# Performance work log

Measured on AMD Instinct MI355X. Metric: run time of the kernel, lower is better.

Reference implementation:

```python
import jax, jax.numpy as jnp
import numpy as np
import math

CLASSES = 1024
IN_F = 32
OUT_F = 32
N = 262144


def setup_inputs() -> dict:
    key = jax.random.key(0)
    k1, k2, k3, k4 = jax.random.split(key, 4)
    k = math.sqrt(1.0 / float(IN_F))
    inp = jax.random.normal(k1, (N, IN_F), dtype=jnp.float32)
    inds = jax.random.randint(k2, (N,), 0, CLASSES, dtype=jnp.int32)
    w = jax.random.uniform(k3, (CLASSES, IN_F, OUT_F), dtype=jnp.float32, minval=-k, maxval=k)
    b = jax.random.uniform(k4, (CLASSES, 1, OUT_F), dtype=jnp.float32, minval=-k, maxval=k)
    return {"input": inp, "inds": inds, "w": w, "b": b}


def reference(input, inds, w, b):
    # per-row expert matmul: out[n] = input[n] @ w[inds[n]] + b[inds[n]]
    w_g = w[inds]            # [n, in, out] gathered expert weights
    b_g = b[inds, 0]         # [n, out]
    return jnp.einsum('ni,nio->no', input, w_g) + b_g
```

## Files before the change

### kernel.cpp

```cpp
#include <hip/hip_runtime.h>


#define N_ROWS      262144
#define N_CLASSES   1024
#define IN_F        32
#define OUT_F       32
#define HB          64
#define ROWS_PER_HB (N_ROWS / HB)

__global__ __launch_bounds__(256) void k_hist(const int* __restrict__ inds,
                                              int* __restrict__ bcT) {
    __shared__ int h[N_CLASSES];
    const int tid = threadIdx.x;
    for (int c = tid; c < N_CLASSES; c += 256) h[c] = 0;
    __syncthreads();
    const int base = blockIdx.x * ROWS_PER_HB;
    for (int k = 0; k < ROWS_PER_HB; k += 256)
        atomicAdd(&h[inds[base + k + tid]], 1);
    __syncthreads();
    for (int c = tid; c < N_CLASSES; c += 256)
        bcT[c * HB + blockIdx.x] = h[c];
}

__global__ __launch_bounds__(1024) void k_scan(const int* __restrict__ bcT,
                                               int* __restrict__ cls_off) {
    __shared__ int s[N_CLASSES];
    const int c = threadIdx.x;
    const int4* p = (const int4*)(bcT + c * HB);
    int total = 0;
#pragma unroll
    for (int j = 0; j < HB / 4; ++j) {
        const int4 t = p[j];
        total += t.x + t.y + t.z + t.w;
    }
    s[c] = total;
    __syncthreads();
    for (int off = 1; off < N_CLASSES; off <<= 1) {
        int v = (c >= off) ? s[c - off] : 0;
        __syncthreads();
        s[c] += v;
        __syncthreads();
    }
    cls_off[c] = s[c] - total;
    if (c == N_CLASSES - 1) cls_off[N_CLASSES] = s[c];
}

__global__ __launch_bounds__(256) void k_offsets(int* __restrict__ bcT,
                                                 const int* __restrict__ cls_off) {
    const int c = blockIdx.x * 256 + threadIdx.x;
    int run = cls_off[c];
    int4* p = (int4*)(bcT + c * HB);
#pragma unroll
    for (int j = 0; j < HB / 4; ++j) {
        const int4 t = p[j];
        int4 o;
        o.x = run; run += t.x;
        o.y = run; run += t.y;
        o.z = run; run += t.z;
        o.w = run; run += t.w;
        p[j] = o;
    }
}

__global__ __launch_bounds__(256) void k_scatter(const int* __restrict__ inds,
                                                 const int* __restrict__ bcT,
                                                 int* __restrict__ rowids) {
    __shared__ int cur[N_CLASSES];
    const int tid = threadIdx.x;
    for (int c = tid; c < N_CLASSES; c += 256)
        cur[c] = bcT[c * HB + blockIdx.x];
    __syncthreads();
    const int base = blockIdx.x * ROWS_PER_HB;
    for (int k = 0; k < ROWS_PER_HB; k += 256) {
        const int row = base + k + tid;
        const int c = inds[row];
        const int pos = atomicAdd(&cur[c], 1);
        rowids[pos] = row;
    }
}

__global__ __launch_bounds__(256) void k_condmul(const float* __restrict__ input,
                                                 const float* __restrict__ w,
                                                 const float* __restrict__ bias,
                                                 const int* __restrict__ rowids,
                                                 const int* __restrict__ cls_off,
                                                 float* __restrict__ out) {
    __shared__ float wlds[IN_F * OUT_F];
    const int cls = blockIdx.x;
    const int tid = threadIdx.x;

    ((float4*)wlds)[tid] = ((const float4*)(w + (size_t)cls * IN_F * OUT_F))[tid];

    const int oq = tid & 7;
    const int rg = tid >> 3;
    const float4 bv = ((const float4*)(bias + (size_t)cls * OUT_F))[oq];
    const int start = cls_off[cls];
    const int count = cls_off[cls + 1] - start;
    __syncthreads();

    const float4* wl4 = (const float4*)wlds;
    const int iters = (count + 31) >> 5;
    for (int it = 0; it < iters; ++it) {
        const int ri = it * 32 + rg;
        const bool valid = ri < count;
        const int idx = valid ? ri : (count - 1);
        const int row = rowids[start + idx];

        const float4* xin = (const float4*)(input + (size_t)row * IN_F);
        float4 x[8];
#pragma unroll
        for (int j = 0; j < 8; ++j) x[j] = xin[j];

        float4 acc = bv;
#pragma unroll
        for (int j = 0; j < 8; ++j) {
            const float a0 = x[j].x, a1 = x[j].y, a2 = x[j].z, a3 = x[j].w;
            const float4 w0 = wl4[(j * 4 + 0) * (OUT_F / 4) + oq];
            const float4 w1 = wl4[(j * 4 + 1) * (OUT_F / 4) + oq];
            const float4 w2 = wl4[(j * 4 + 2) * (OUT_F / 4) + oq];
            const float4 w3 = wl4[(j * 4 + 3) * (OUT_F / 4) + oq];
            acc.x += a0 * w0.x; acc.y += a0 * w0.y; acc.z += a0 * w0.z; acc.w += a0 * w0.w;
            acc.x += a1 * w1.x; acc.y += a1 * w1.y; acc.z += a1 * w1.z; acc.w += a1 * w1.w;
            acc.x += a2 * w2.x; acc.y += a2 * w2.y; acc.z += a2 * w2.z; acc.w += a2 * w2.w;
            acc.x += a3 * w3.x; acc.y += a3 * w3.y; acc.z += a3 * w3.z; acc.w += a3 * w3.w;
        }
        if (valid)
            ((float4*)(out + (size_t)row * OUT_F))[oq] = acc;
    }
}

__global__ __launch_bounds__(256) void k_naive(const float* __restrict__ input,
                                               const int* __restrict__ inds,
                                               const float* __restrict__ w,
                                               const float* __restrict__ bias,
                                               float* __restrict__ out) {
    const int tid = threadIdx.x;
    const int oq = tid & 7;
    const int rg = tid >> 3;
    const int row = blockIdx.x * 32 + rg;
    if (row >= N_ROWS) return;
    const int c = inds[row];
    const float4* xin = (const float4*)(input + (size_t)row * IN_F);
    const float4* wr = (const float4*)(w + (size_t)c * IN_F * OUT_F);
    float4 acc = ((const float4*)(bias + (size_t)c * OUT_F))[oq];
#pragma unroll
    for (int j = 0; j < 8; ++j) {
        const float4 xv = xin[j];
        const float a0 = xv.x, a1 = xv.y, a2 = xv.z, a3 = xv.w;
        const float4 w0 = wr[(j * 4 + 0) * (OUT_F / 4) + oq];
        const float4 w1 = wr[(j * 4 + 1) * (OUT_F / 4) + oq];
        const float4 w2 = wr[(j * 4 + 2) * (OUT_F / 4) + oq];
        const float4 w3 = wr[(j * 4 + 3) * (OUT_F / 4) + oq];
        acc.x += a0 * w0.x; acc.y += a0 * w0.y; acc.z += a0 * w0.z; acc.w += a0 * w0.w;
        acc.x += a1 * w1.x; acc.y += a1 * w1.y; acc.z += a1 * w1.z; acc.w += a1 * w1.w;
        acc.x += a2 * w2.x; acc.y += a2 * w2.y; acc.z += a2 * w2.z; acc.w += a2 * w2.w;
        acc.x += a3 * w3.x; acc.y += a3 * w3.y; acc.z += a3 * w3.z; acc.w += a3 * w3.w;
    }
    ((float4*)(out + (size_t)row * OUT_F))[oq] = acc;
}

extern "C" void kernel_launch(void* const* d_in, const int* in_sizes, int n_in,
                              void* d_out, int out_size, void* d_ws, size_t ws_size,
                              hipStream_t stream) {
    const float* input = (const float*)d_in[0];
    const int*   inds  = (const int*)d_in[1];
    const float* w     = (const float*)d_in[2];
    const float* bias  = (const float*)d_in[3];
    float* out = (float*)d_out;

    int* ws = (int*)d_ws;
    int* bcT     = ws;
    int* cls_off = ws + N_CLASSES * HB;
    int* rowids  = cls_off + N_CLASSES + 1 + 3;
    const size_t need = (size_t)(N_CLASSES * HB + N_CLASSES + 4 + N_ROWS) * sizeof(int);

    if (ws_size >= need) {
        k_hist<<<HB, 256, 0, stream>>>(inds, bcT);
        k_scan<<<1, 1024, 0, stream>>>(bcT, cls_off);
        k_offsets<<<N_CLASSES / 256, 256, 0, stream>>>(bcT, cls_off);
        k_scatter<<<HB, 256, 0, stream>>>(inds, bcT, rowids);
        k_condmul<<<N_CLASSES, 256, 0, stream>>>(input, w, bias, rowids, cls_off, out);
    } else {
        k_naive<<<N_ROWS / 32, 256, 0, stream>>>(input, inds, w, bias, out);
    }
}
```

Measured before the change: 125.2 us.

## Hold expert weights in registers and split the K dimension across thread pairs

The per-class matmul kernel now keeps each thread's slice of the expert weights (16 float4) in registers instead of staging the whole matrix in LDS. The input dimension is split into two halves across thread pairs, with the partial sums combined by a cross-lane shuffle, and the block size doubles to 512 with an occupancy hint. This removes the LDS weight reads and the block barrier from the inner loop. In exchange it raises register pressure, makes redundant global weight loads per thread, and each shuffle adds a cross-lane exchange per row.

```diff
diff --git a/kernel.cpp b/kernel.cpp
--- a/kernel.cpp
+++ b/kernel.cpp
@@ -79,26 +79,29 @@
     }
 }
 
-__global__ __launch_bounds__(256) void k_condmul(const float* __restrict__ input,
-                                                 const float* __restrict__ w,
-                                                 const float* __restrict__ bias,
-                                                 const int* __restrict__ rowids,
-                                                 const int* __restrict__ cls_off,
-                                                 float* __restrict__ out) {
-    __shared__ float wlds[IN_F * OUT_F];
+__global__ __launch_bounds__(512, 4) void k_condmul(const float* __restrict__ input,
+                                                    const float* __restrict__ w,
+                                                    const float* __restrict__ bias,
+                                                    const int* __restrict__ rowids,
+                                                    const int* __restrict__ cls_off,
+                                                    float* __restrict__ out) {
     const int cls = blockIdx.x;
     const int tid = threadIdx.x;
-
-    ((float4*)wlds)[tid] = ((const float4*)(w + (size_t)cls * IN_F * OUT_F))[tid];
-
     const int oq = tid & 7;
-    const int rg = tid >> 3;
-    const float4 bv = ((const float4*)(bias + (size_t)cls * OUT_F))[oq];
+    const int kh = (tid >> 3) & 1;
+    const int rg = tid >> 4;
+
     const int start = cls_off[cls];
     const int count = cls_off[cls + 1] - start;
-    __syncthreads();
-
-    const float4* wl4 = (const float4*)wlds;
+    if (count <= 0) return;
+
+    const float4* w4 = (const float4*)(w + (size_t)cls * (IN_F * OUT_F)) + (size_t)kh * 16 * (OUT_F / 4) + oq;
+    float4 wk[16];
+#pragma unroll
+    for (int j = 0; j < 16; ++j) wk[j] = w4[(size_t)j * (OUT_F / 4)];
+
+    const float4 bv = ((const float4*)(bias + (size_t)cls * OUT_F))[oq];
+
     const int iters = (count + 31) >> 5;
     for (int it = 0; it < iters; ++it) {
         const int ri = it * 32 + rg;
@@ -106,26 +109,37 @@
         const int idx = valid ? ri : (count - 1);
         const int row = rowids[start + idx];
 
-        const float4* xin = (const float4*)(input + (size_t)row * IN_F);
-        float4 x[8];
-#pragma unroll
-        for (int j = 0; j < 8; ++j) x[j] = xin[j];
-
-        float4 acc = bv;
-#pragma unroll
-        for (int j = 0; j < 8; ++j) {
+        const float4* xin = (const float4*)(input + (size_t)row * IN_F + kh * 16);
+        float4 x[4];
+#pragma unroll
+        for (int j = 0; j < 4; ++j) x[j] = xin[j];
+
+        float4 acc = {0.f, 0.f, 0.f, 0.f};
+#pragma unroll
+        for (int j = 0; j < 4; ++j) {
             const float a0 = x[j].x, a1 = x[j].y, a2 = x[j].z, a3 = x[j].w;
-            const float4 w0 = wl4[(j * 4 + 0) * (OUT_F / 4) + oq];
-            const float4 w1 = wl4[(j * 4 + 1) * (OUT_F / 4) + oq];
-            const float4 w2 = wl4[(j * 4 + 2) * (OUT_F / 4) + oq];
-            const float4 w3 = wl4[(j * 4 + 3) * (OUT_F / 4) + oq];
+            const float4 w0 = wk[4 * j + 0];
+            const float4 w1 = wk[4 * j + 1];
+            const float4 w2 = wk[4 * j + 2];
+            const float4 w3 = wk[4 * j + 3];
             acc.x += a0 * w0.x; acc.y += a0 * w0.y; acc.z += a0 * w0.z; acc.w += a0 * w0.w;
             acc.x += a1 * w1.x; acc.y += a1 * w1.y; acc.z += a1 * w1.z; acc.w += a1 * w1.w;
             acc.x += a2 * w2.x; acc.y += a2 * w2.y; acc.z += a2 * w2.z; acc.w += a2 * w2.w;
             acc.x += a3 * w3.x; acc.y += a3 * w3.y; acc.z += a3 * w3.z; acc.w += a3 * w3.w;
         }
-        if (valid)
-            ((float4*)(out + (size_t)row * OUT_F))[oq] = acc;
+        acc.x += __shfl_xor(acc.x, 8);
+        acc.y += __shfl_xor(acc.y, 8);
+        acc.z += __shfl_xor(acc.z, 8);
+        acc.w += __shfl_xor(acc.w, 8);
+
+        if (valid && kh == 0) {
+            float4 o;
+            o.x = acc.x + bv.x;
+            o.y = acc.y + bv.y;
+            o.z = acc.z + bv.z;
+            o.w = acc.w + bv.w;
+            ((float4*)(out + (size_t)row * OUT_F))[oq] = o;
+        }
     }
 }
 
@@ -179,7 +193,7 @@
         k_scan<<<1, 1024, 0, stream>>>(bcT, cls_off);
         k_offsets<<<N_CLASSES / 256, 256, 0, stream>>>(bcT, cls_off);
         k_scatter<<<HB, 256, 0, stream>>>(inds, bcT, rowids);
-        k_condmul<<<N_CLASSES, 256, 0, stream>>>(input, w, bias, rowids, cls_off, out);
+        k_condmul<<<N_CLASSES, 512, 0, stream>>>(input, w, bias, rowids, cls_off, out);
     } else {
         k_naive<<<N_ROWS / 32, 256, 0, stream>>>(input, inds, w, bias, out);
     }
```

Measured after the change: 138.6 us. +10.7%, slower.

## Fuse offsets pass into scan kernel and process two rows per thread

Applied to the files above, without the earlier changes.

Folds the per-block offset computation into the single-block scan kernel, which removes one kernel launch. The condmul kernel now handles two rows per thread per iteration so loads and FMAs from independent rows can overlap, reusing each LDS weight read twice. It also adds an early exit for empty classes. In exchange the fused offset pass runs on one block of 1024 threads instead of four blocks, and register pressure goes up.

```diff
diff --git a/kernel.cpp b/kernel.cpp
--- a/kernel.cpp
+++ b/kernel.cpp
@@ -22,11 +22,11 @@
         bcT[c * HB + blockIdx.x] = h[c];
 }
 
-__global__ __launch_bounds__(1024) void k_scan(const int* __restrict__ bcT,
+__global__ __launch_bounds__(1024) void k_scan(int* __restrict__ bcT,
                                                int* __restrict__ cls_off) {
     __shared__ int s[N_CLASSES];
     const int c = threadIdx.x;
-    const int4* p = (const int4*)(bcT + c * HB);
+    int4* p = (int4*)(bcT + c * HB);
     int total = 0;
 #pragma unroll
     for (int j = 0; j < HB / 4; ++j) {
@@ -41,15 +41,9 @@
         s[c] += v;
         __syncthreads();
     }
-    cls_off[c] = s[c] - total;
+    int run = s[c] - total;
+    cls_off[c] = run;
     if (c == N_CLASSES - 1) cls_off[N_CLASSES] = s[c];
-}
-
-__global__ __launch_bounds__(256) void k_offsets(int* __restrict__ bcT,
-                                                 const int* __restrict__ cls_off) {
-    const int c = blockIdx.x * 256 + threadIdx.x;
-    int run = cls_off[c];
-    int4* p = (int4*)(bcT + c * HB);
 #pragma unroll
     for (int j = 0; j < HB / 4; ++j) {
         const int4 t = p[j];
@@ -88,44 +82,55 @@
     __shared__ float wlds[IN_F * OUT_F];
     const int cls = blockIdx.x;
     const int tid = threadIdx.x;
-
     ((float4*)wlds)[tid] = ((const float4*)(w + (size_t)cls * IN_F * OUT_F))[tid];
 
     const int oq = tid & 7;
     const int rg = tid >> 3;
-    const float4 bv = ((const float4*)(bias + (size_t)cls * OUT_F))[oq];
     const int start = cls_off[cls];
     const int count = cls_off[cls + 1] - start;
+    const float4 bv = ((const float4*)(bias + (size_t)cls * OUT_F))[oq];
     __syncthreads();
+    if (count <= 0) return;
 
     const float4* wl4 = (const float4*)wlds;
-    const int iters = (count + 31) >> 5;
+    const int iters = (count + 63) >> 6;
     for (int it = 0; it < iters; ++it) {
-        const int ri = it * 32 + rg;
-        const bool valid = ri < count;
-        const int idx = valid ? ri : (count - 1);
-        const int row = rowids[start + idx];
+        const int riA = it * 64 + rg;
+        const int riB = riA + 32;
+        const bool va = riA < count;
+        const bool vb = riB < count;
+        const int rowA = rowids[start + (va ? riA : count - 1)];
+        const int rowB = rowids[start + (vb ? riB : count - 1)];
 
-        const float4* xin = (const float4*)(input + (size_t)row * IN_F);
-        float4 x[8];
+        const float4* xa4 = (const float4*)(input + (size_t)rowA * IN_F);
+        const float4* xb4 = (const float4*)(input + (size_t)rowB * IN_F);
+        float4 xa[8], xb[8];
 #pragma unroll
-        for (int j = 0; j < 8; ++j) x[j] = xin[j];
+        for (int j = 0; j < 8; ++j) xa[j] = xa4[j];
+#pragma unroll
+        for (int j = 0; j < 8; ++j) xb[j] = xb4[j];
 
-        float4 acc = bv;
+        float4 accA = bv;
+        float4 accB = bv;
 #pragma unroll
         for (int j = 0; j < 8; ++j) {
-            const float a0 = x[j].x, a1 = x[j].y, a2 = x[j].z, a3 = x[j].w;
+            const float a0 = xa[j].x, a1 = xa[j].y, a2 = xa[j].z, a3 = xa[j].w;
+            const float b0 = xb[j].x, b1 = xb[j].y, b2 = xb[j].z, b3 = xb[j].w;
             const float4 w0 = wl4[(j * 4 + 0) * (OUT_F / 4) + oq];
             const float4 w1 = wl4[(j * 4 + 1) * (OUT_F / 4) + oq];
             const float4 w2 = wl4[(j * 4 + 2) * (OUT_F / 4) + oq];
             const float4 w3 = wl4[(j * 4 + 3) * (OUT_F / 4) + oq];
-            acc.x += a0 * w0.x; acc.y += a0 * w0.y; acc.z += a0 * w0.z; acc.w += a0 * w0.w;
-            acc.x += a1 * w1.x; acc.y += a1 * w1.y; acc.z += a1 * w1.z; acc.w += a1 * w1.w;
-            acc.x += a2 * w2.x; acc.y += a2 * w2.y; acc.z += a2 * w2.z; acc.w += a2 * w2.w;
-            acc.x += a3 * w3.x; acc.y += a3 * w3.y; acc.z += a3 * w3.z; acc.w += a3 * w3.w;
+            accA.x += a0 * w0.x; accA.y += a0 * w0.y; accA.z += a0 * w0.z; accA.w += a0 * w0.w;
+            accA.x += a1 * w1.x; accA.y += a1 * w1.y; accA.z += a1 * w1.z; accA.w += a1 * w1.w;
+            accA.x += a2 * w2.x; accA.y += a2 * w2.y; accA.z += a2 * w2.z; accA.w += a2 * w2.w;
+            accA.x += a3 * w3.x; accA.y += a3 * w3.y; accA.z += a3 * w3.z; accA.w += a3 * w3.w;
+            accB.x += b0 * w0.x; accB.y += b0 * w0.y; accB.z += b0 * w0.z; accB.w += b0 * w0.w;
+            accB.x += b1 * w1.x; accB.y += b1 * w1.y; accB.z += b1 * w1.z; accB.w += b1 * w1.w;
+            accB.x += b2 * w2.x; accB.y += b2 * w2.y; accB.z += b2 * w2.z; accB.w += b2 * w2.w;
+            accB.x += b3 * w3.x; accB.y += b3 * w3.y; accB.z += b3 * w3.z; accB.w += b3 * w3.w;
         }
-        if (valid)
-            ((float4*)(out + (size_t)row * OUT_F))[oq] = acc;
+        if (va) ((float4*)(out + (size_t)rowA * OUT_F))[oq] = accA;
+        if (vb) ((float4*)(out + (size_t)rowB * OUT_F))[oq] = accB;
     }
 }
 
@@ -177,7 +182,6 @@
     if (ws_size >= need) {
         k_hist<<<HB, 256, 0, stream>>>(inds, bcT);
         k_scan<<<1, 1024, 0, stream>>>(bcT, cls_off);
-        k_offsets<<<N_CLASSES / 256, 256, 0, stream>>>(bcT, cls_off);
         k_scatter<<<HB, 256, 0, stream>>>(inds, bcT, rowids);
         k_condmul<<<N_CLASSES, 256, 0, stream>>>(input, w, bias, rowids, cls_off, out);
     } else {
```

After: 146.2 us. 16.8% more time.
